# Optimization experiments

Measured on AMD Instinct MI355X. Metric: run time of the kernel, lower is better.

The kernel has to match this reference:

```python
import jax, jax.numpy as jnp
import numpy as np

F = 128   # flattened observation features
H = 64    # MLP/LSTM hidden size (hardcoded in module)
A = 15    # number of discrete actions
T = 128   # rollout length (timesteps)
B = 2048  # number of parallel envs (batch)


def setup_inputs() -> dict:
    key = jax.random.key(0)
    ks = jax.random.split(key, 12)
    n = lambda k, sh, s=1.0: jax.random.normal(k, sh, jnp.float32) * s
    return {
        "x": n(ks[0], (T * B, F)),
        "done": (jax.random.uniform(ks[1], (T * B,)) < 0.05).astype(jnp.float32),
        "h0": n(ks[2], (1, B, H)),
        "c0": n(ks[3], (1, B, H)),
        # MLP encoder params (Linear stores y = x @ W + b here, W: [in, out])
        "W1": n(ks[4], (F, H), 0.1), "b1": jnp.zeros((H,), jnp.float32),
        "W2": n(ks[5], (H, H), 0.1), "b2": jnp.zeros((H,), jnp.float32),
        # LSTM params, PyTorch layout: weight_ih [4H, H_in], gate order i,f,g,o
        "Wih": n(ks[6], (4 * H, H), 0.1), "bih": jnp.zeros((4 * H,), jnp.float32),
        "Whh": n(ks[7], (4 * H, H), 0.1), "bhh": jnp.zeros((4 * H,), jnp.float32),
        # actor / critic heads
        "Wa": n(ks[8], (H, A), 0.01), "ba": jnp.zeros((A,), jnp.float32),
        "Wc": n(ks[9], (H, 1), 1.0), "bc": jnp.zeros((1,), jnp.float32),
    }


def reference(x, done, h0, c0, W1, b1, W2, b2, Wih, bih, Whh, bhh, Wa, ba, Wc, bc):
    Bsz, Hh = h0.shape[1], h0.shape[2]
    # MLP encoder: Linear -> Tanh -> Linear -> Tanh
    y = jnp.tanh(x @ W1 + b1)
    y = jnp.tanh(y @ W2 + b2)                 # [T*B, H]
    y = y.reshape(-1, Bsz, Hh)                # [T, B, H]
    d = done.reshape(-1, Bsz)                 # [T, B]

    def step(carry, td):
        h, c = carry
        yt, dt = td
        m = (1.0 - dt)[:, None]               # done-mask hidden reset
        h = h * m
        c = c * m
        g = yt @ Wih.T + bih + h @ Whh.T + bhh  # [B, 4H]
        i, f, gg, o = jnp.split(g, 4, axis=-1)
        c = jax.nn.sigmoid(f) * c + jax.nn.sigmoid(i) * jnp.tanh(gg)
        h = jax.nn.sigmoid(o) * jnp.tanh(c)
        return (h, c), h

    (hT, cT), outs = jax.lax.scan(step, (h0[0], c0[0]), (y, d))
    z = outs.reshape(-1, Hh)                  # [T*B, H]
    logits = z @ Wa + ba                      # Categorical logits
    vf = z @ Wc + bc
    return logits, vf, hT[None], cT[None]
```

## Files before the change

kernel.cpp:

```cpp
#include <hip/hip_runtime.h>
#include <hip/hip_bf16.h>
#include <stdint.h>

typedef __bf16  bf16x8 __attribute__((ext_vector_type(8)));
typedef short   s16x8  __attribute__((ext_vector_type(8)));
typedef int     i32x4  __attribute__((ext_vector_type(4)));
typedef float   f32x4  __attribute__((ext_vector_type(4)));

union Frag { s16x8 s; bf16x8 b; i32x4 i; };

static __device__ __forceinline__ short f2bf(float f) {
    union { float f; unsigned u; } v; v.f = f;
    unsigned r = (v.u + 0x7FFFu + ((v.u >> 16) & 1u)) >> 16;
    return (short)r;
}
static __device__ __forceinline__ float bf2f(short s) {
    union { unsigned u; float f; } v; v.u = ((unsigned)(unsigned short)s) << 16;
    return v.f;
}
static __device__ __forceinline__ float fast_rcp(float x) { return __builtin_amdgcn_rcpf(x); }
static __device__ __forceinline__ float sigm(float x) { return fast_rcp(1.0f + __expf(-x)); }
static __device__ __forceinline__ float tanh_fast(float x) {
    float e = __expf(-2.0f * x);
    return (1.0f - e) * fast_rcp(1.0f + e);
}
static __device__ __forceinline__ f32x4 mfma16(bf16x8 a, bf16x8 b, f32x4 c) {
    return __builtin_amdgcn_mfma_f32_16x16x32_bf16(a, b, c, 0, 0, 0);
}

static __device__ __forceinline__ void block_sync_lds() {
    asm volatile("s_waitcnt lgkmcnt(0)\n\ts_barrier" ::: "memory");
}

#define GLDS(gp, lp) __builtin_amdgcn_global_load_lds( \
    (const __attribute__((address_space(1))) void*)(gp), \
    (__attribute__((address_space(3))) void*)(lp), 16, 0, 0)

#define TT 128
#define BB 2048
#define HH 64
#define FF 128
#define AA 15
#define CH 8
#define LOGITS_OFF 0
#define VF_OFF   3932160
#define HT_OFF   4194304
#define CT_OFF   4325376


__global__ __launch_bounds__(256) void enc_kernel(
    const float* __restrict__ x, const float* __restrict__ W1, const float* __restrict__ b1,
    const float* __restrict__ W2, const float* __restrict__ b2, short* __restrict__ y_sw)
{
    __shared__ short w1t[64][136];
    __shared__ short w2t[64][72];
    __shared__ short c1buf[4][16][72];
    __shared__ short ybuf[4][16][72];

    const int tid  = threadIdx.x;
    const int lane = tid & 63;
    const int w    = tid >> 6;
    const int c    = lane & 15;
    const int q    = lane >> 4;

    for (int i = tid; i < 128*64; i += 256) { int k = i >> 6, n = i & 63; w1t[n][k] = f2bf(W1[i]); }
    for (int i = tid; i < 64*64;  i += 256) { int k = i >> 6, n = i & 63; w2t[n][k] = f2bf(W2[i]); }

    float b1v[4], b2v[4];
#pragma unroll
    for (int ct = 0; ct < 4; ++ct) { b1v[ct] = b1[16*ct + c]; b2v[ct] = b2[16*ct + c]; }
    __syncthreads();

    for (int it = 0; it < 4; ++it) {
        const int wt = it*4096 + blockIdx.x*4 + w;
        const int r0 = wt * 16;
        Frag af[4];
#pragma unroll
        for (int kf = 0; kf < 4; ++kf) {
            const float* xp = x + (size_t)(r0 + c)*FF + 32*kf + 8*q;
            f32x4 x0 = *(const f32x4*)xp;
            f32x4 x1 = *(const f32x4*)(xp + 4);
#pragma unroll
            for (int jj = 0; jj < 4; ++jj) { af[kf].s[jj] = f2bf(x0[jj]); af[kf].s[4+jj] = f2bf(x1[jj]); }
        }
        f32x4 acc[4];
#pragma unroll
        for (int ct = 0; ct < 4; ++ct) acc[ct] = (f32x4){b1v[ct], b1v[ct], b1v[ct], b1v[ct]};
#pragma unroll
        for (int kf = 0; kf < 4; ++kf)
#pragma unroll
            for (int ct = 0; ct < 4; ++ct) {
                Frag bf; bf.s = *(const s16x8*)&w1t[16*ct + c][32*kf + 8*q];
                acc[ct] = mfma16(af[kf].b, bf.b, acc[ct]);
            }
#pragma unroll
        for (int ct = 0; ct < 4; ++ct)
#pragma unroll
            for (int i = 0; i < 4; ++i)
                c1buf[w][4*q + i][16*ct + c] = f2bf(tanh_fast(acc[ct][i]));
        Frag a2[2];
#pragma unroll
        for (int kf = 0; kf < 2; ++kf) a2[kf].s = *(const s16x8*)&c1buf[w][c][32*kf + 8*q];
        f32x4 acc2[4];
#pragma unroll
        for (int ct = 0; ct < 4; ++ct) acc2[ct] = (f32x4){b2v[ct], b2v[ct], b2v[ct], b2v[ct]};
#pragma unroll
        for (int kf = 0; kf < 2; ++kf)
#pragma unroll
            for (int ct = 0; ct < 4; ++ct) {
                Frag bf; bf.s = *(const s16x8*)&w2t[16*ct + c][32*kf + 8*q];
                acc2[ct] = mfma16(a2[kf].b, bf.b, acc2[ct]);
            }
#pragma unroll
        for (int ct = 0; ct < 4; ++ct)
#pragma unroll
            for (int i = 0; i < 4; ++i)
                ybuf[w][4*q + i][16*ct + c] = f2bf(tanh_fast(acc2[ct][i]));
        {
            const int kf2 = lane >> 5;
            const int c8  = (lane >> 2) & 7;
            const int qq  = lane & 3;
#pragma unroll
            for (int g = 0; g < 2; ++g) {
                s16x8 yv = *(const s16x8*)&ybuf[w][c8 + 8*g][32*kf2 + 8*qq];
                *(s16x8*)(y_sw + ((size_t)(wt >> 7)*256 + (size_t)(wt & 127)*2 + g)*512 + lane*8) = yv;
            }
        }
    }
}

__global__ __launch_bounds__(512, 1) void scan_kernel(
    const short* __restrict__ y_sw, const float* __restrict__ done,
    const float* __restrict__ h0, const float* __restrict__ c0,
    const float* __restrict__ Wih, const float* __restrict__ bih,
    const float* __restrict__ Whh, const float* __restrict__ bhh,
    const float* __restrict__ Wa, const float* __restrict__ ba,
    const float* __restrict__ Wc, const float* __restrict__ bc,
    float* __restrict__ out_logits, float* __restrict__ out_vf,
    float* __restrict__ hT_out, float* __restrict__ cT_out)
{
    __shared__ short ybuf[2][CH][512];
    __shared__ float obuf[2][CH][8][16];
    __shared__ short zbuf[2][8][72];
    __shared__ short hbuf[2][8][72];
    __shared__ float dbuf[TT+1][8];

    const int tid  = threadIdx.x;
    const int lane = tid & 63;
    const int w    = tid >> 6;
    const int c    = lane & 15;
    const int q    = lane >> 4;
    const int blk  = blockIdx.x;
    const int b0   = blk * 8;
    const bool crit = (w < 4);
    const int hw   = w - 4;
    const int r0   = 4*(q & 1) + 2*(q >> 1);

    Frag  wf[4][2];
    Frag  wfi[4][2];
    float biasv[4];
    Frag  hwf[2];
    float hbv = 0.f;
    float cst0 = 0.f, cst1 = 0.f;
    f32x4 gyr[4];

    if (crit) {
        const int jcol = 16*w + c;
#pragma unroll
        for (int a = 0; a < 4; ++a) {
            const int col = 64*a + jcol;
            biasv[a] = bih[col] + bhh[col];
#pragma unroll
            for (int kf = 0; kf < 2; ++kf) {
                const float* wp = Whh + (size_t)col*HH + 32*kf + 8*q;
                f32x4 w0 = *(const f32x4*)wp;
                f32x4 w1 = *(const f32x4*)(wp + 4);
#pragma unroll
                for (int jj = 0; jj < 4; ++jj) { wf[a][kf].s[jj] = f2bf(w0[jj]); wf[a][kf].s[4+jj] = f2bf(w1[jj]); }
                const float* vp = Wih + (size_t)col*HH + 32*kf + 8*q;
                f32x4 v0 = *(const f32x4*)vp;
                f32x4 v1 = *(const f32x4*)(vp + 4);
#pragma unroll
                for (int jj = 0; jj < 4; ++jj) { wfi[a][kf].s[jj] = f2bf(v0[jj]); wfi[a][kf].s[4+jj] = f2bf(v1[jj]); }
            }
        }
    } else {
#pragma unroll
        for (int kf = 0; kf < 2; ++kf)
#pragma unroll
            for (int jj = 0; jj < 8; ++jj) {
                int k = 32*kf + 8*q + jj;
                hwf[kf].s[jj] = f2bf((c < 15) ? Wa[k*AA + c] : Wc[k]);
            }
        hbv = (c < 15) ? ba[c] : bc[0];
        {
            const int t0 = hw * 32;
            const float* gp = done + (size_t)(t0 + (lane >> 1))*BB + b0 + 4*(lane & 1);
            GLDS(gp, &dbuf[t0][0]);
        }
#pragma unroll
        for (int i = 0; i < 2; ++i) {
            const int ss = hw*2 + i;
            const short* gp = y_sw + ((size_t)ss*256 + blk)*512 + lane*8;
            GLDS(gp, &ybuf[0][ss][0]);
        }
        __builtin_amdgcn_s_waitcnt(0x0F70);
    }
    if (tid < 8) dbuf[TT][tid] = 0.0f;
    __syncthreads();

    if (crit) {
        const int jcol = 16*w + c;
        {
            float d0 = dbuf[0][r0 + 0];
            float d1 = dbuf[0][r0 + 1];
            float cv0 = c0[(size_t)(b0 + r0 + 0)*HH + jcol];
            float cv1 = c0[(size_t)(b0 + r0 + 1)*HH + jcol];
            cst0 = (d0 != 0.0f) ? 0.0f : cv0;
            cst1 = (d1 != 0.0f) ? 0.0f : cv1;
        }
        if (tid < 128) {
            int mm = tid & 7, j4 = (tid >> 3) & 15;
            float dm = dbuf[0][mm];
            f32x4 hv = *(const f32x4*)(h0 + (size_t)(b0 + mm)*HH + 4*j4);
#pragma unroll
            for (int ii = 0; ii < 4; ++ii)
                hbuf[0][mm][4*j4 + ii] = (dm != 0.0f) ? (short)0 : f2bf(hv[ii]);
        }
        {
            Frag yc0, yc1;
            yc0.s = *(const s16x8*)&ybuf[0][0][((c & 7)*4 + q)*8];
            yc1.s = *(const s16x8*)&ybuf[0][0][(32 + (c & 7)*4 + q)*8];
#pragma unroll
            for (int a = 0; a < 4; ++a) {
                f32x4 g = (f32x4){biasv[a], biasv[a], biasv[a], biasv[a]};
                g = mfma16(yc0.b, wfi[a][0].b, g);
                g = mfma16(yc1.b, wfi[a][1].b, g);
                gyr[a] = g;
            }
        }
    }
    __syncthreads();

    for (int t = 0; t < TT; ++t) {
        if (crit) {
            const int jcol = 16*w + c;
            const int cur = t & 1;
            Frag hf0, hf1;
            hf0.s = *(const s16x8*)&hbuf[cur][c & 7][8*q];
            hf1.s = *(const s16x8*)&hbuf[cur][c & 7][32 + 8*q];
            f32x4 acc[4];
#pragma unroll
            for (int a = 0; a < 4; ++a) {
                acc[a] = mfma16(hf0.b, wf[a][0].b, gyr[a]);
                acc[a] = mfma16(hf1.b, wf[a][1].b, acc[a]);
            }
            const bool hiq = (q >= 2);
            float g0[4], g1[4];
#pragma unroll
            for (int a = 0; a < 4; ++a) {
                g0[a] = hiq ? acc[a][2] : acc[a][0];
                g1[a] = hiq ? acc[a][3] : acc[a][1];
            }
            const float dn0 = dbuf[t+1][r0 + 0];
            const float dn1 = dbuf[t+1][r0 + 1];
            if (t < TT-1) {
                const int tn = t + 1;
                const int ch = (tn >> 3) & 1, sl = tn & 7;
                Frag yc0, yc1;
                yc0.s = *(const s16x8*)&ybuf[ch][sl][((c & 7)*4 + q)*8];
                yc1.s = *(const s16x8*)&ybuf[ch][sl][(32 + (c & 7)*4 + q)*8];
#pragma unroll
                for (int a = 0; a < 4; ++a) {
                    f32x4 g = (f32x4){biasv[a], biasv[a], biasv[a], biasv[a]};
                    g = mfma16(yc0.b, wfi[a][0].b, g);
                    g = mfma16(yc1.b, wfi[a][1].b, g);
                    gyr[a] = g;
                }
            }
#define ELEM(GV, CSTV, RI, DN) {                                        \
            float ei = __expf(-GV[0]), ef = __expf(-GV[1]);             \
            float eg = __expf(-2.0f*GV[2]), eo = __expf(-GV[3]);        \
            float term = (1.0f - eg) * fast_rcp((1.0f + ei)*(1.0f + eg)); \
            float cn = fast_rcp(1.0f + ef)*CSTV + term;                 \
            float ec = __expf(-2.0f*cn);                                \
            float hv = (1.0f - ec) * fast_rcp((1.0f + eo)*(1.0f + ec)); \
            short zb = f2bf(hv);                                        \
            zbuf[cur][RI][jcol] = zb;                                   \
            const bool d = ((DN) != 0.0f);                              \
            CSTV = d ? 0.0f : cn;                                       \
            hbuf[cur ^ 1][RI][jcol] = d ? (short)0 : zb; }
            ELEM(g0, cst0, r0 + 0, dn0)
            ELEM(g1, cst1, r0 + 1, dn1)
#undef ELEM
        } else {
            if ((t & 7) == 0 && t < 120) {
                const int k = (t >> 3) + 1;
#pragma unroll
                for (int i = 0; i < 2; ++i) {
                    const int ss = hw*2 + i;
                    const short* gp = y_sw + ((size_t)(8*k + ss)*256 + blk)*512 + lane*8;
                    GLDS(gp, &ybuf[k & 1][ss][0]);
                }
            }
            if ((t & 7) == 1 && t > 8 && w == 4) {
                const int cc = (t >> 3) - 1;
                const int s = lane >> 3, r = lane & 7;
                const size_t row = (size_t)(8*cc + s)*BB + b0 + r;
                const float* ob = &obuf[cc & 1][s][r][0];
                float* lp = out_logits + row*AA;
#pragma unroll
                for (int n = 0; n < 15; ++n) lp[n] = ob[n];
                out_vf[row] = ob[15];
            }
            if (t >= 1 && w == 4 + ((t + 2) & 3)) {
                const int tp = t - 1;
                Frag zf0, zf1;
                zf0.s = *(const s16x8*)&zbuf[tp & 1][c & 7][8*q];
                zf1.s = *(const s16x8*)&zbuf[tp & 1][c & 7][32 + 8*q];
                f32x4 ha = (f32x4){hbv, hbv, hbv, hbv};
                ha = mfma16(zf0.b, hwf[0].b, ha);
                ha = mfma16(zf1.b, hwf[1].b, ha);
                if (q < 2) {
#pragma unroll
                    for (int i = 0; i < 4; ++i)
                        obuf[(tp >> 3) & 1][tp & 7][4*q + i][c] = ha[i];
                }
            }
            if ((t & 7) == 6)
                __builtin_amdgcn_s_waitcnt(0x0F70);
        }
        block_sync_lds();
    }

    if (!crit && w == 7) {
        Frag zf0, zf1;
        zf0.s = *(const s16x8*)&zbuf[1][c & 7][8*q];
        zf1.s = *(const s16x8*)&zbuf[1][c & 7][32 + 8*q];
        f32x4 ha = (f32x4){hbv, hbv, hbv, hbv};
        ha = mfma16(zf0.b, hwf[0].b, ha);
        ha = mfma16(zf1.b, hwf[1].b, ha);
        if (q < 2) {
#pragma unroll
            for (int i = 0; i < 4; ++i) obuf[1][7][4*q + i][c] = ha[i];
        }
    }
    __syncthreads();
    if (!crit && w == 4) {
        const int s = lane >> 3, r = lane & 7;
        const size_t row = (size_t)(120 + s)*BB + b0 + r;
        const float* ob = &obuf[1][s][r][0];
        float* lp = out_logits + row*AA;
#pragma unroll
        for (int n = 0; n < 15; ++n) lp[n] = ob[n];
        out_vf[row] = ob[15];
    }
    if (tid < 128) {
        int mm = tid & 7, j4 = (tid >> 3) & 15;
        f32x4 hv;
#pragma unroll
        for (int ii = 0; ii < 4; ++ii) hv[ii] = bf2f(zbuf[1][mm][4*j4 + ii]);
        *(f32x4*)(hT_out + (size_t)(b0 + mm)*HH + 4*j4) = hv;
    }
    if (crit) {
        const int jcol = 16*w + c;
        cT_out[(size_t)(b0 + r0 + 0)*HH + jcol] = cst0;
        cT_out[(size_t)(b0 + r0 + 1)*HH + jcol] = cst1;
    }
}

extern "C" void kernel_launch(void* const* d_in, const int* in_sizes, int n_in,
                              void* d_out, int out_size, void* d_ws, size_t ws_size,
                              hipStream_t stream) {
    const float* x    = (const float*)d_in[0];
    const float* done = (const float*)d_in[1];
    const float* h0   = (const float*)d_in[2];
    const float* c0   = (const float*)d_in[3];
    const float* W1   = (const float*)d_in[4];
    const float* b1   = (const float*)d_in[5];
    const float* W2   = (const float*)d_in[6];
    const float* b2   = (const float*)d_in[7];
    const float* Wih  = (const float*)d_in[8];
    const float* bih  = (const float*)d_in[9];
    const float* Whh  = (const float*)d_in[10];
    const float* bhh  = (const float*)d_in[11];
    const float* Wa   = (const float*)d_in[12];
    const float* ba   = (const float*)d_in[13];
    const float* Wc   = (const float*)d_in[14];
    const float* bc   = (const float*)d_in[15];
    float* out = (float*)d_out;

    short* y_sw = (short*)d_ws;

    enc_kernel<<<1024, 256, 0, stream>>>(x, W1, b1, W2, b2, y_sw);
    scan_kernel<<<256, 512, 0, stream>>>(y_sw, done, h0, c0, Wih, bih, Whh, bhh,
                                         Wa, ba, Wc, bc,
                                         out + LOGITS_OFF, out + VF_OFF,
                                         out + HT_OFF, out + CT_OFF);
}
```

Before: 295.0 us.

## Fuse MLP encoder into LSTM scan kernel, computed by idle helper waves

Removes the separate encoder kernel and its bf16 workspace round-trip. The four non-critical waves in each scan block now load x and run the two-layer MLP for the next 8-timestep chunk, spread over the 8 steps of the current chunk, writing straight into LDS. This removes a kernel launch and the global write/read of y, but adds MLP work and x loads to the helper waves inside the serial step loop. That could lengthen per-step barrier time if the helpers become the critical path.

```diff
diff --git a/kernel.cpp b/kernel.cpp
--- a/kernel.cpp
+++ b/kernel.cpp
@@ -19,7 +19,6 @@
     return v.f;
 }
 static __device__ __forceinline__ float fast_rcp(float x) { return __builtin_amdgcn_rcpf(x); }
-static __device__ __forceinline__ float sigm(float x) { return fast_rcp(1.0f + __expf(-x)); }
 static __device__ __forceinline__ float tanh_fast(float x) {
     float e = __expf(-2.0f * x);
     return (1.0f - e) * fast_rcp(1.0f + e);
@@ -47,91 +46,77 @@
 #define HT_OFF   4194304
 #define CT_OFF   4325376
 
-
-__global__ __launch_bounds__(256) void enc_kernel(
-    const float* __restrict__ x, const float* __restrict__ W1, const float* __restrict__ b1,
-    const float* __restrict__ W2, const float* __restrict__ b2, short* __restrict__ y_sw)
+static __device__ __forceinline__ void xload(
+    const float* __restrict__ x, int t_x, int b0, int lane, int q, f32x4* xr)
 {
-    __shared__ short w1t[64][136];
-    __shared__ short w2t[64][72];
-    __shared__ short c1buf[4][16][72];
-    __shared__ short ybuf[4][16][72];
-
-    const int tid  = threadIdx.x;
-    const int lane = tid & 63;
-    const int w    = tid >> 6;
-    const int c    = lane & 15;
-    const int q    = lane >> 4;
-
-    for (int i = tid; i < 128*64; i += 256) { int k = i >> 6, n = i & 63; w1t[n][k] = f2bf(W1[i]); }
-    for (int i = tid; i < 64*64;  i += 256) { int k = i >> 6, n = i & 63; w2t[n][k] = f2bf(W2[i]); }
-
-    float b1v[4], b2v[4];
-#pragma unroll
-    for (int ct = 0; ct < 4; ++ct) { b1v[ct] = b1[16*ct + c]; b2v[ct] = b2[16*ct + c]; }
-    __syncthreads();
-
-    for (int it = 0; it < 4; ++it) {
-        const int wt = it*4096 + blockIdx.x*4 + w;
-        const int r0 = wt * 16;
-        Frag af[4];
-#pragma unroll
-        for (int kf = 0; kf < 4; ++kf) {
-            const float* xp = x + (size_t)(r0 + c)*FF + 32*kf + 8*q;
-            f32x4 x0 = *(const f32x4*)xp;
-            f32x4 x1 = *(const f32x4*)(xp + 4);
-#pragma unroll
-            for (int jj = 0; jj < 4; ++jj) { af[kf].s[jj] = f2bf(x0[jj]); af[kf].s[4+jj] = f2bf(x1[jj]); }
-        }
-        f32x4 acc[4];
-#pragma unroll
-        for (int ct = 0; ct < 4; ++ct) acc[ct] = (f32x4){b1v[ct], b1v[ct], b1v[ct], b1v[ct]};
-#pragma unroll
-        for (int kf = 0; kf < 4; ++kf)
-#pragma unroll
-            for (int ct = 0; ct < 4; ++ct) {
-                Frag bf; bf.s = *(const s16x8*)&w1t[16*ct + c][32*kf + 8*q];
-                acc[ct] = mfma16(af[kf].b, bf.b, acc[ct]);
-            }
+    const float* xp = x + ((size_t)t_x*BB + b0 + (lane & 7))*FF + 8*q;
+#pragma unroll
+    for (int kf = 0; kf < 4; ++kf) {
+        xr[2*kf]   = *(const f32x4*)(xp + 32*kf);
+        xr[2*kf+1] = *(const f32x4*)(xp + 32*kf + 4);
+    }
+}
+static __device__ __forceinline__ void mlp_l1(
+    const f32x4* xr, const float* b1v, const short (*w1t)[136],
+    int c, int q, f32x4* acc1)
+{
+    Frag af[4];
+#pragma unroll
+    for (int kf = 0; kf < 4; ++kf)
+#pragma unroll
+        for (int jj = 0; jj < 4; ++jj) {
+            af[kf].s[jj]   = f2bf(xr[2*kf][jj]);
+            af[kf].s[4+jj] = f2bf(xr[2*kf+1][jj]);
+        }
+#pragma unroll
+    for (int ct = 0; ct < 4; ++ct) acc1[ct] = (f32x4){b1v[ct], b1v[ct], b1v[ct], b1v[ct]};
+#pragma unroll
+    for (int kf = 0; kf < 4; ++kf)
+#pragma unroll
+        for (int ct = 0; ct < 4; ++ct) {
+            Frag bf; bf.s = *(const s16x8*)&w1t[16*ct + c][32*kf + 8*q];
+            acc1[ct] = mfma16(af[kf].b, bf.b, acc1[ct]);
+        }
+}
+static __device__ __forceinline__ void mlp_mid(
+    const f32x4* acc1, short (*c1)[72], int c, int q, Frag* a2f)
+{
+    if (q < 2)
 #pragma unroll
         for (int ct = 0; ct < 4; ++ct)
 #pragma unroll
             for (int i = 0; i < 4; ++i)
-                c1buf[w][4*q + i][16*ct + c] = f2bf(tanh_fast(acc[ct][i]));
-        Frag a2[2];
-#pragma unroll
-        for (int kf = 0; kf < 2; ++kf) a2[kf].s = *(const s16x8*)&c1buf[w][c][32*kf + 8*q];
-        f32x4 acc2[4];
-#pragma unroll
-        for (int ct = 0; ct < 4; ++ct) acc2[ct] = (f32x4){b2v[ct], b2v[ct], b2v[ct], b2v[ct]};
-#pragma unroll
-        for (int kf = 0; kf < 2; ++kf)
-#pragma unroll
-            for (int ct = 0; ct < 4; ++ct) {
-                Frag bf; bf.s = *(const s16x8*)&w2t[16*ct + c][32*kf + 8*q];
-                acc2[ct] = mfma16(a2[kf].b, bf.b, acc2[ct]);
-            }
+                c1[4*q + i][16*ct + c] = f2bf(tanh_fast(acc1[ct][i]));
+    a2f[0].s = *(const s16x8*)&c1[c & 7][8*q];
+    a2f[1].s = *(const s16x8*)&c1[c & 7][32 + 8*q];
+}
+static __device__ __forceinline__ void mlp_l2(
+    const Frag* a2f, const float* b2v, const short (*w2t)[72],
+    short (*yout)[72], int c, int q)
+{
+    f32x4 acc2[4];
+#pragma unroll
+    for (int ct = 0; ct < 4; ++ct) acc2[ct] = (f32x4){b2v[ct], b2v[ct], b2v[ct], b2v[ct]};
+#pragma unroll
+    for (int kf = 0; kf < 2; ++kf)
+#pragma unroll
+        for (int ct = 0; ct < 4; ++ct) {
+            Frag bf; bf.s = *(const s16x8*)&w2t[16*ct + c][32*kf + 8*q];
+            acc2[ct] = mfma16(a2f[kf].b, bf.b, acc2[ct]);
+        }
+    if (q < 2)
 #pragma unroll
         for (int ct = 0; ct < 4; ++ct)
 #pragma unroll
             for (int i = 0; i < 4; ++i)
-                ybuf[w][4*q + i][16*ct + c] = f2bf(tanh_fast(acc2[ct][i]));
-        {
-            const int kf2 = lane >> 5;
-            const int c8  = (lane >> 2) & 7;
-            const int qq  = lane & 3;
-#pragma unroll
-            for (int g = 0; g < 2; ++g) {
-                s16x8 yv = *(const s16x8*)&ybuf[w][c8 + 8*g][32*kf2 + 8*qq];
-                *(s16x8*)(y_sw + ((size_t)(wt >> 7)*256 + (size_t)(wt & 127)*2 + g)*512 + lane*8) = yv;
-            }
-        }
-    }
-}
-
-__global__ __launch_bounds__(512, 1) void scan_kernel(
-    const short* __restrict__ y_sw, const float* __restrict__ done,
+                yout[4*q + i][16*ct + c] = f2bf(tanh_fast(acc2[ct][i]));
+}
+
+__global__ __launch_bounds__(512, 1) void fused_kernel(
+    const float* __restrict__ x, const float* __restrict__ done,
     const float* __restrict__ h0, const float* __restrict__ c0,
+    const float* __restrict__ W1, const float* __restrict__ b1,
+    const float* __restrict__ W2, const float* __restrict__ b2,
     const float* __restrict__ Wih, const float* __restrict__ bih,
     const float* __restrict__ Whh, const float* __restrict__ bhh,
     const float* __restrict__ Wa, const float* __restrict__ ba,
@@ -139,7 +124,10 @@
     float* __restrict__ out_logits, float* __restrict__ out_vf,
     float* __restrict__ hT_out, float* __restrict__ cT_out)
 {
-    __shared__ short ybuf[2][CH][512];
+    __shared__ short w1t[64][136];
+    __shared__ short w2t[64][72];
+    __shared__ short ybuf[2][CH][8][72];
+    __shared__ short c1buf[4][8][72];
     __shared__ float obuf[2][CH][8][16];
     __shared__ short zbuf[2][8][72];
     __shared__ short hbuf[2][8][72];
@@ -161,8 +149,15 @@
     float biasv[4];
     Frag  hwf[2];
     float hbv = 0.f;
+    float b1v[4] = {0,0,0,0}, b2v[4] = {0,0,0,0};
     float cst0 = 0.f, cst1 = 0.f;
     f32x4 gyr[4];
+    f32x4 xr[8];
+    f32x4 acc1[4];
+    Frag  a2f[2];
+
+    for (int i = tid; i < 128*64; i += 512) { int k = i >> 6, n = i & 63; w1t[n][k] = f2bf(W1[i]); }
+    for (int i = tid; i < 64*64;  i += 512) { int k = i >> 6, n = i & 63; w2t[n][k] = f2bf(W2[i]); }
 
     if (crit) {
         const int jcol = 16*w + c;
@@ -185,6 +180,11 @@
             }
         }
     } else {
+        {
+            const int t0 = hw * 32;
+            const float* gp = done + (size_t)(t0 + (lane >> 1))*BB + b0 + 4*(lane & 1);
+            GLDS(gp, &dbuf[t0][0]);
+        }
 #pragma unroll
         for (int kf = 0; kf < 2; ++kf)
 #pragma unroll
@@ -193,21 +193,24 @@
                 hwf[kf].s[jj] = f2bf((c < 15) ? Wa[k*AA + c] : Wc[k]);
             }
         hbv = (c < 15) ? ba[c] : bc[0];
-        {
-            const int t0 = hw * 32;
-            const float* gp = done + (size_t)(t0 + (lane >> 1))*BB + b0 + 4*(lane & 1);
-            GLDS(gp, &dbuf[t0][0]);
-        }
-#pragma unroll
-        for (int i = 0; i < 2; ++i) {
-            const int ss = hw*2 + i;
-            const short* gp = y_sw + ((size_t)ss*256 + blk)*512 + lane*8;
-            GLDS(gp, &ybuf[0][ss][0]);
-        }
+#pragma unroll
+        for (int ct = 0; ct < 4; ++ct) { b1v[ct] = b1[16*ct + c]; b2v[ct] = b2[16*ct + c]; }
+        xload(x, 2*hw + 0, b0, lane, q, xr);
+    }
+    if (tid < 8) dbuf[TT][tid] = 0.0f;
+    block_sync_lds();
+
+    if (!crit) {
+        mlp_l1(xr, b1v, w1t, c, q, acc1);
+        mlp_mid(acc1, c1buf[hw], c, q, a2f);
+        mlp_l2(a2f, b2v, w2t, ybuf[0][2*hw + 0], c, q);
+        xload(x, 2*hw + 1, b0, lane, q, xr);
+        mlp_l1(xr, b1v, w1t, c, q, acc1);
+        mlp_mid(acc1, c1buf[hw], c, q, a2f);
+        mlp_l2(a2f, b2v, w2t, ybuf[0][2*hw + 1], c, q);
         __builtin_amdgcn_s_waitcnt(0x0F70);
     }
-    if (tid < 8) dbuf[TT][tid] = 0.0f;
-    __syncthreads();
+    block_sync_lds();
 
     if (crit) {
         const int jcol = 16*w + c;
@@ -229,8 +232,8 @@
         }
         {
             Frag yc0, yc1;
-            yc0.s = *(const s16x8*)&ybuf[0][0][((c & 7)*4 + q)*8];
-            yc1.s = *(const s16x8*)&ybuf[0][0][(32 + (c & 7)*4 + q)*8];
+            yc0.s = *(const s16x8*)&ybuf[0][0][lane & 7][8*q];
+            yc1.s = *(const s16x8*)&ybuf[0][0][lane & 7][32 + 8*q];
 #pragma unroll
             for (int a = 0; a < 4; ++a) {
                 f32x4 g = (f32x4){biasv[a], biasv[a], biasv[a], biasv[a]};
@@ -240,103 +243,106 @@
             }
         }
     }
-    __syncthreads();
-
-    for (int t = 0; t < TT; ++t) {
-        if (crit) {
-            const int jcol = 16*w + c;
-            const int cur = t & 1;
-            Frag hf0, hf1;
-            hf0.s = *(const s16x8*)&hbuf[cur][c & 7][8*q];
-            hf1.s = *(const s16x8*)&hbuf[cur][c & 7][32 + 8*q];
-            f32x4 acc[4];
-#pragma unroll
-            for (int a = 0; a < 4; ++a) {
-                acc[a] = mfma16(hf0.b, wf[a][0].b, gyr[a]);
-                acc[a] = mfma16(hf1.b, wf[a][1].b, acc[a]);
+    block_sync_lds();
+
+    for (int tc = 0; tc < 16; ++tc) {
+#pragma unroll
+        for (int p = 0; p < 8; ++p) {
+            const int t = 8*tc + p;
+            if (crit) {
+                const int jcol = 16*w + c;
+                const int cur = p & 1;
+                Frag hf0, hf1;
+                hf0.s = *(const s16x8*)&hbuf[cur][lane & 7][8*q];
+                hf1.s = *(const s16x8*)&hbuf[cur][lane & 7][32 + 8*q];
+                f32x4 acc[4];
+#pragma unroll
+                for (int a = 0; a < 4; ++a) {
+                    acc[a] = mfma16(hf0.b, wf[a][0].b, gyr[a]);
+                    acc[a] = mfma16(hf1.b, wf[a][1].b, acc[a]);
+                }
+                const bool hiq = (q >= 2);
+                float g0[4], g1[4];
+#pragma unroll
+                for (int a = 0; a < 4; ++a) {
+                    g0[a] = hiq ? acc[a][2] : acc[a][0];
+                    g1[a] = hiq ? acc[a][3] : acc[a][1];
+                }
+                const float dn0 = dbuf[t+1][r0 + 0];
+                const float dn1 = dbuf[t+1][r0 + 1];
+                if (tc < 15 || p < 7) {
+                    const int ch = (p < 7) ? (tc & 1) : ((tc + 1) & 1);
+                    const int sl = (p + 1) & 7;
+                    Frag yc0, yc1;
+                    yc0.s = *(const s16x8*)&ybuf[ch][sl][lane & 7][8*q];
+                    yc1.s = *(const s16x8*)&ybuf[ch][sl][lane & 7][32 + 8*q];
+#pragma unroll
+                    for (int a = 0; a < 4; ++a) {
+                        f32x4 g = (f32x4){biasv[a], biasv[a], biasv[a], biasv[a]};
+                        g = mfma16(yc0.b, wfi[a][0].b, g);
+                        g = mfma16(yc1.b, wfi[a][1].b, g);
+                        gyr[a] = g;
+                    }
+                }
+#define ELEM(GV, CSTV, RI, DN) {                                        \
+                float ei = __expf(-GV[0]), ef = __expf(-GV[1]);         \
+                float eg = __expf(-2.0f*GV[2]), eo = __expf(-GV[3]);    \
+                float term = (1.0f - eg) * fast_rcp((1.0f + ei)*(1.0f + eg)); \
+                float cn = fast_rcp(1.0f + ef)*CSTV + term;             \
+                float ec = __expf(-2.0f*cn);                            \
+                float hv = (1.0f - ec) * fast_rcp((1.0f + eo)*(1.0f + ec)); \
+                short zb = f2bf(hv);                                    \
+                zbuf[cur][RI][jcol] = zb;                               \
+                const bool d = ((DN) != 0.0f);                          \
+                CSTV = d ? 0.0f : cn;                                   \
+                hbuf[cur ^ 1][RI][jcol] = d ? (short)0 : zb; }
+                ELEM(g0, cst0, r0 + 0, dn0)
+                ELEM(g1, cst1, r0 + 1, dn1)
+#undef ELEM
+            } else {
+                if (p == 0 && tc < 15) xload(x, 8*(tc+1) + 2*hw + 0, b0, lane, q, xr);
+                if (p == 1 && tc < 15) mlp_l1(xr, b1v, w1t, c, q, acc1);
+                if (p == 2 && tc < 15) {
+                    xload(x, 8*(tc+1) + 2*hw + 1, b0, lane, q, xr);
+                    mlp_mid(acc1, c1buf[hw], c, q, a2f);
+                }
+                if (p == 3 && tc < 15) mlp_l2(a2f, b2v, w2t, ybuf[(tc+1) & 1][2*hw + 0], c, q);
+                if (p == 4 && tc < 15) mlp_l1(xr, b1v, w1t, c, q, acc1);
+                if (p == 5 && tc < 15) mlp_mid(acc1, c1buf[hw], c, q, a2f);
+                if (p == 6 && tc < 15) mlp_l2(a2f, b2v, w2t, ybuf[(tc+1) & 1][2*hw + 1], c, q);
+                if (p == 7 && tc >= 1 && w == 4) {
+                    const int cc = tc - 1;
+                    const int s = lane >> 3, r = lane & 7;
+                    const size_t row = (size_t)(8*cc + s)*BB + b0 + r;
+                    const float* ob = &obuf[cc & 1][s][r][0];
+                    float* lp = out_logits + row*AA;
+#pragma unroll
+                    for (int n = 0; n < 15; ++n) lp[n] = ob[n];
+                    out_vf[row] = ob[15];
+                }
+                if ((tc > 0 || p > 0) && w == 4 + (p & 3)) {
+                    const int tp = t - 1;
+                    Frag zf0, zf1;
+                    zf0.s = *(const s16x8*)&zbuf[tp & 1][lane & 7][8*q];
+                    zf1.s = *(const s16x8*)&zbuf[tp & 1][lane & 7][32 + 8*q];
+                    f32x4 ha = (f32x4){hbv, hbv, hbv, hbv};
+                    ha = mfma16(zf0.b, hwf[0].b, ha);
+                    ha = mfma16(zf1.b, hwf[1].b, ha);
+                    if (q < 2) {
+#pragma unroll
+                        for (int i = 0; i < 4; ++i)
+                            obuf[(tp >> 3) & 1][tp & 7][4*q + i][c] = ha[i];
+                    }
+                }
             }
-            const bool hiq = (q >= 2);
-            float g0[4], g1[4];
-#pragma unroll
-            for (int a = 0; a < 4; ++a) {
-                g0[a] = hiq ? acc[a][2] : acc[a][0];
-                g1[a] = hiq ? acc[a][3] : acc[a][1];
-            }
-            const float dn0 = dbuf[t+1][r0 + 0];
-            const float dn1 = dbuf[t+1][r0 + 1];
-            if (t < TT-1) {
-                const int tn = t + 1;
-                const int ch = (tn >> 3) & 1, sl = tn & 7;
-                Frag yc0, yc1;
-                yc0.s = *(const s16x8*)&ybuf[ch][sl][((c & 7)*4 + q)*8];
-                yc1.s = *(const s16x8*)&ybuf[ch][sl][(32 + (c & 7)*4 + q)*8];
-#pragma unroll
-                for (int a = 0; a < 4; ++a) {
-                    f32x4 g = (f32x4){biasv[a], biasv[a], biasv[a], biasv[a]};
-                    g = mfma16(yc0.b, wfi[a][0].b, g);
-                    g = mfma16(yc1.b, wfi[a][1].b, g);
-                    gyr[a] = g;
-                }
-            }
-#define ELEM(GV, CSTV, RI, DN) {                                        \
-            float ei = __expf(-GV[0]), ef = __expf(-GV[1]);             \
-            float eg = __expf(-2.0f*GV[2]), eo = __expf(-GV[3]);        \
-            float term = (1.0f - eg) * fast_rcp((1.0f + ei)*(1.0f + eg)); \
-            float cn = fast_rcp(1.0f + ef)*CSTV + term;                 \
-            float ec = __expf(-2.0f*cn);                                \
-            float hv = (1.0f - ec) * fast_rcp((1.0f + eo)*(1.0f + ec)); \
-            short zb = f2bf(hv);                                        \
-            zbuf[cur][RI][jcol] = zb;                                   \
-            const bool d = ((DN) != 0.0f);                              \
-            CSTV = d ? 0.0f : cn;                                       \
-            hbuf[cur ^ 1][RI][jcol] = d ? (short)0 : zb; }
-            ELEM(g0, cst0, r0 + 0, dn0)
-            ELEM(g1, cst1, r0 + 1, dn1)
-#undef ELEM
-        } else {
-            if ((t & 7) == 0 && t < 120) {
-                const int k = (t >> 3) + 1;
-#pragma unroll
-                for (int i = 0; i < 2; ++i) {
-                    const int ss = hw*2 + i;
-                    const short* gp = y_sw + ((size_t)(8*k + ss)*256 + blk)*512 + lane*8;
-                    GLDS(gp, &ybuf[k & 1][ss][0]);
-                }
-            }
-            if ((t & 7) == 1 && t > 8 && w == 4) {
-                const int cc = (t >> 3) - 1;
-                const int s = lane >> 3, r = lane & 7;
-                const size_t row = (size_t)(8*cc + s)*BB + b0 + r;
-                const float* ob = &obuf[cc & 1][s][r][0];
-                float* lp = out_logits + row*AA;
-#pragma unroll
-                for (int n = 0; n < 15; ++n) lp[n] = ob[n];
-                out_vf[row] = ob[15];
-            }
-            if (t >= 1 && w == 4 + ((t + 2) & 3)) {
-                const int tp = t - 1;
-                Frag zf0, zf1;
-                zf0.s = *(const s16x8*)&zbuf[tp & 1][c & 7][8*q];
-                zf1.s = *(const s16x8*)&zbuf[tp & 1][c & 7][32 + 8*q];
-                f32x4 ha = (f32x4){hbv, hbv, hbv, hbv};
-                ha = mfma16(zf0.b, hwf[0].b, ha);
-                ha = mfma16(zf1.b, hwf[1].b, ha);
-                if (q < 2) {
-#pragma unroll
-                    for (int i = 0; i < 4; ++i)
-                        obuf[(tp >> 3) & 1][tp & 7][4*q + i][c] = ha[i];
-                }
-            }
-            if ((t & 7) == 6)
-                __builtin_amdgcn_s_waitcnt(0x0F70);
-        }
-        block_sync_lds();
+            block_sync_lds();
+        }
     }
 
     if (!crit && w == 7) {
         Frag zf0, zf1;
-        zf0.s = *(const s16x8*)&zbuf[1][c & 7][8*q];
-        zf1.s = *(const s16x8*)&zbuf[1][c & 7][32 + 8*q];
+        zf0.s = *(const s16x8*)&zbuf[1][lane & 7][8*q];
+        zf1.s = *(const s16x8*)&zbuf[1][lane & 7][32 + 8*q];
         f32x4 ha = (f32x4){hbv, hbv, hbv, hbv};
         ha = mfma16(zf0.b, hwf[0].b, ha);
         ha = mfma16(zf1.b, hwf[1].b, ha);
@@ -390,11 +396,10 @@
     const float* bc   = (const float*)d_in[15];
     float* out = (float*)d_out;
 
-    short* y_sw = (short*)d_ws;
-
-    enc_kernel<<<1024, 256, 0, stream>>>(x, W1, b1, W2, b2, y_sw);
-    scan_kernel<<<256, 512, 0, stream>>>(y_sw, done, h0, c0, Wih, bih, Whh, bhh,
-                                         Wa, ba, Wc, bc,
-                                         out + LOGITS_OFF, out + VF_OFF,
-                                         out + HT_OFF, out + CT_OFF);
-}
+    (void)d_ws; (void)ws_size;
+
+    fused_kernel<<<256, 512, 0, stream>>>(x, done, h0, c0, W1, b1, W2, b2,
+                                          Wih, bih, Whh, bhh, Wa, ba, Wc, bc,
+                                          out + LOGITS_OFF, out + VF_OFF,
+                                          out + HT_OFF, out + CT_OFF);
+}
```

Result: no change. 297.8 us (+1.0%).
